# Optimization experiments

Measured on AMD Instinct MI355X. Metric: run time of the kernel, lower is better.

Reference implementation:

```python
import jax, jax.numpy as jnp
import numpy as np

B, C, H, W = 32, 128, 32, 32
E, K, D, HID = 16, 2, 128, 512  # nbExperts, topK, nbIn=nbOut, hidden=4*max(nbIn,nbOut)


def setup_inputs() -> dict:
    key = jax.random.key(0)
    ks = jax.random.split(key, 6)
    init = lambda k, shape, fan: (jax.random.normal(k, shape, jnp.float32) / np.sqrt(fan)).astype(jnp.float32)
    return {
        "x": jax.random.normal(ks[0], (B, C, H, W), jnp.float32),
        "gate_w": init(ks[1], (D, E), D),
        "gate_b": jnp.zeros((E,), jnp.float32),
        "noise_w": init(ks[2], (D, E), D),
        "noise_b": jnp.zeros((E,), jnp.float32),
        "w1": init(ks[3], (E, D, HID), D),
        "b1": jnp.zeros((E, HID), jnp.float32),
        "w2": init(ks[4], (E, HID, D), HID),
        "b2": jnp.zeros((E, D), jnp.float32),
        "top_k": K,
    }


def reference(x, gate_w, gate_b, noise_w, noise_b, w1, b1, w2, b2, top_k):
    b, c, h, w = x.shape
    xt = x.transpose(0, 2, 3, 1).reshape(-1, c)  # [T, D] tokens (fromCNN path)
    T = xt.shape[0]

    # --- GatingWithNoise: gate(x) + randn * softplus(noise(x)) ---
    logits = xt @ gate_w + gate_b                      # [T, E]
    noise_sd = jax.nn.softplus(xt @ noise_w + noise_b)  # [T, E]
    noise = jax.random.normal(jax.random.key(42), logits.shape, logits.dtype)
    logits = logits + noise * noise_sd

    # --- top-k, softmax over k, scatter to dense [T, E] gate matrix ---
    top_vals, top_idx = jax.lax.top_k(logits, top_k)   # [T, K]
    probs = jax.nn.softmax(top_vals, axis=1)           # [T, K]
    gates = jnp.zeros((T, E), x.dtype).at[jnp.arange(T)[:, None], top_idx].set(probs)

    # --- dense path: run every expert, weighted combine ---
    hdn = jax.nn.relu(jnp.einsum('td,edh->teh', xt, w1) + b1)  # [T, E, HID]
    eo = jnp.einsum('teh,ehd->ted', hdn, w2) + b2              # [T, E, D]
    out = jnp.einsum('te,ted->td', gates, eo)                  # [T, D]

    out = out.reshape(b, h, w, c).transpose(0, 3, 1, 2)        # back to NCHW
    gates = gates.reshape(b, h, w, E)
    return out, gates
```

## Files before the change

### kernel.cpp

```cpp
#include <hip/hip_runtime.h>
#include <stdint.h>

#define NB       32
#define NC       128
#define NHW      1024
#define NT       32768
#define NE       16
#define NHID     512
#define NGBLK    512

typedef __attribute__((ext_vector_type(8))) short short8v;
typedef __attribute__((ext_vector_type(4))) float f32x4;

__device__ __forceinline__ unsigned short f2bf(float f) {
    uint32_t u = __float_as_uint(f);
    uint32_t r = u + 0x7fffu + ((u >> 16) & 1u);
    return (unsigned short)(r >> 16);
}
__device__ __forceinline__ float bf2f(unsigned short u) {
    return __uint_as_float(((uint32_t)u) << 16);
}

__device__ __forceinline__ void gll16(const void* g, void* l) {
    __builtin_amdgcn_global_load_lds(
        (const __attribute__((address_space(1))) uint32_t*)g,
        (__attribute__((address_space(3))) uint32_t*)l, 16, 0, 0);
}

#define WAIT_VM4_LGKM0() asm volatile("s_waitcnt vmcnt(4) lgkmcnt(0)" ::: "memory")
#define WAIT_VM0_LGKM0() asm volatile("s_waitcnt vmcnt(0) lgkmcnt(0)" ::: "memory")
#define WAIT_LGKM()      asm volatile("s_waitcnt lgkmcnt(0)" ::: "memory")
#define SBAR()           { asm volatile("" ::: "memory"); __builtin_amdgcn_s_barrier(); asm volatile("" ::: "memory"); }

__device__ __forceinline__ uint32_t rotl32(uint32_t x, uint32_t d) {
    return (x << d) | (x >> (32u - d));
}

__device__ __forceinline__ void threefry2x32_20(uint32_t k0, uint32_t k1,
                                                uint32_t& x0, uint32_t& x1) {
    const uint32_t ks0 = k0, ks1 = k1, ks2 = k0 ^ k1 ^ 0x1BD11BDAu;
    x0 += ks0; x1 += ks1;
#define TFR(r) { x0 += x1; x1 = rotl32(x1, r); x1 ^= x0; }
    TFR(13u) TFR(15u) TFR(26u) TFR(6u)
    x0 += ks1; x1 += ks2 + 1u;
    TFR(17u) TFR(29u) TFR(16u) TFR(24u)
    x0 += ks2; x1 += ks0 + 2u;
    TFR(13u) TFR(15u) TFR(26u) TFR(6u)
    x0 += ks0; x1 += ks1 + 3u;
    TFR(17u) TFR(29u) TFR(16u) TFR(24u)
    x0 += ks1; x1 += ks2 + 4u;
    TFR(13u) TFR(15u) TFR(26u) TFR(6u)
    x0 += ks2; x1 += ks0 + 5u;
#undef TFR
}

__device__ __forceinline__ float erfinv_xla_f32(float x) {
    float w = -log1pf(-x * x);
    float p;
    if (w < 5.0f) {
        w = w - 2.5f;
        p = 2.81022636e-08f;
        p = fmaf(p, w, 3.43273939e-07f);
        p = fmaf(p, w, -3.5233877e-06f);
        p = fmaf(p, w, -4.39150654e-06f);
        p = fmaf(p, w, 0.00021858087f);
        p = fmaf(p, w, -0.00125372503f);
        p = fmaf(p, w, -0.00417768164f);
        p = fmaf(p, w, 0.246640727f);
        p = fmaf(p, w, 1.50140941f);
    } else {
        w = sqrtf(w) - 3.0f;
        p = -0.000200214257f;
        p = fmaf(p, w, 0.000100950558f);
        p = fmaf(p, w, 0.00134934322f);
        p = fmaf(p, w, -0.00367342844f);
        p = fmaf(p, w, 0.00573950773f);
        p = fmaf(p, w, -0.0076224613f);
        p = fmaf(p, w, 0.00943887047f);
        p = fmaf(p, w, 1.00167406f);
        p = fmaf(p, w, 2.83297682f);
    }
    return p * x;
}

__device__ __forceinline__ float jax_noise_elem(uint32_t i) {
    uint32_t x0 = 0u, x1 = i;
    threefry2x32_20(0u, 42u, x0, x1);
    uint32_t bits = x0 ^ x1;
    float f = __uint_as_float(0x3f800000u | (bits >> 9)) - 1.0f;
    const float lo = -0.99999994f;
    float u = f * 2.0f + lo;
    u = fmaxf(lo, u);
    return 1.41421354f * erfinv_xla_f32(u);
}

__global__ __launch_bounds__(256) void moe_gate_tw_kernel(
    const float* __restrict__ x,
    const float* __restrict__ gate_w, const float* __restrict__ gate_b,
    const float* __restrict__ noise_w, const float* __restrict__ noise_b,
    float* __restrict__ gates_out,
    int*   __restrict__ top_idx,
    float* __restrict__ top_prob,
    int*   __restrict__ rank,
    int*   __restrict__ bcnt,
    unsigned short* __restrict__ xtb,
    const float* __restrict__ w1, unsigned short* __restrict__ w1bt,
    const float* __restrict__ w2, unsigned short* __restrict__ w2bt,
    int do_new)
{
    __shared__ union { float lw[32 * 160]; float ts[64][65]; } sm;
    __shared__ int lcnt[16];

    const int tid = threadIdx.x;

    if (blockIdx.x >= NGBLK) {
        int blk = blockIdx.x - NGBLK;
        const float* src;  unsigned short* dst;  int R, C;
        if (blk < 256) { src = w1; dst = w1bt; R = 128; C = 512; }
        else           { src = w2; dst = w2bt; R = 512; C = 128; blk -= 256; }
        const int nr = R >> 6, ncc = C >> 6;
        const int e = blk / (nr * ncc);
        const int rem = blk % (nr * ncc);
        const int rt = rem / ncc, ct = rem % ncc;
        const float* S = src + (size_t)e * R * C + (size_t)(rt * 64) * C + ct * 64;
        unsigned short* D = dst + (size_t)e * R * C + (size_t)(ct * 64) * R + rt * 64;
        #pragma unroll
        for (int i = 0; i < 16; ++i) {
            int lin = i * 256 + tid;
            int r = lin >> 6, c = lin & 63;
            sm.ts[r][c] = S[(size_t)r * C + c];
        }
        __syncthreads();
        #pragma unroll
        for (int i = 0; i < 16; ++i) {
            int lin = i * 256 + tid;
            int c = lin >> 6, r = lin & 63;
            D[(size_t)c * R + r] = f2bf(sm.ts[r][c]);
        }
        return;
    }

    const int tl  = tid >> 2;
    const int q   = tid & 3;
    const int t   = blockIdx.x * 64 + tl;
    const int b   = t >> 10, hw = t & 1023;

    if (tid < 16) lcnt[tid] = 0;

    for (int idx = tid; idx < 4096; idx += 256) {
        int ci = idx >> 7;
        int r  = idx & 127;
        int qq = r >> 5, e = r & 31;
        int c  = qq * 32 + ci;
        float v = (e < 16) ? gate_w[c * 16 + e] : noise_w[c * 16 + (e - 16)];
        sm.lw[ci * 160 + qq * 40 + e] = v;
    }
    __syncthreads();

    float acc[32];
    #pragma unroll
    for (int e = 0; e < 32; ++e) acc[e] = 0.f;

    unsigned short xh[32];
    const float* xq = x + (size_t)b * (NC * NHW) + (size_t)(q * 32) * NHW + hw;
    const float* wq = sm.lw + q * 40;
    #pragma unroll 4
    for (int ci = 0; ci < 32; ++ci) {
        float xv = xq[(size_t)ci << 10];
        xh[ci] = f2bf(xv);
        const f32x4* wr = (const f32x4*)(wq + ci * 160);
        #pragma unroll
        for (int j = 0; j < 8; ++j) {
            f32x4 w4 = wr[j];
            #pragma unroll
            for (int k = 0; k < 4; ++k)
                acc[j * 4 + k] = fmaf(xv, w4[k], acc[j * 4 + k]);
        }
    }

    if (do_new) {
        #pragma unroll
        for (int j = 0; j < 4; ++j) {
            short8v v;
            #pragma unroll
            for (int k = 0; k < 8; ++k) v[k] = (short)xh[j * 8 + k];
            *(short8v*)(xtb + (size_t)t * 128 + q * 32 + j * 8) = v;
        }
    }

    #pragma unroll
    for (int e = 0; e < 32; ++e) {
        acc[e] += __shfl_xor(acc[e], 1);
        acc[e] += __shfl_xor(acc[e], 2);
    }

    float lg[4];
    #pragma unroll
    for (int j = 0; j < 4; ++j) {
        int e = q * 4 + j;
        float g  = acc[e] + gate_b[e];
        float an = acc[16 + e] + noise_b[e];
        float sd = fmaxf(an, 0.f) + log1pf(expf(-fabsf(an)));
        float nz = jax_noise_elem((uint32_t)t * 16u + (uint32_t)e);
        lg[j] = fmaf(nz, sd, g);
    }

    float v1 = lg[0], v2 = -INFINITY;
    int   i1 = q * 4, i2 = 0x7fffffff;
    #pragma unroll
    for (int j = 1; j < 4; ++j) {
        float v = lg[j]; int e = q * 4 + j;
        if (v > v1) { v2 = v1; i2 = i1; v1 = v; i1 = e; }
        else if (v > v2) { v2 = v; i2 = e; }
    }
    #pragma unroll
    for (int m = 1; m <= 2; m <<= 1) {
        float pv1 = __shfl_xor(v1, m), pv2 = __shfl_xor(v2, m);
        int   pi1 = __shfl_xor(i1, m), pi2 = __shfl_xor(i2, m);
        bool pBest = (pv1 > v1) || (pv1 == v1 && pi1 < i1);
        float c2v; int c2i;
        if (pBest) { c2v = v1;  c2i = i1;  v1 = pv1; i1 = pi1;
                     if (!((c2v > pv2) || (c2v == pv2 && c2i < pi2))) { c2v = pv2; c2i = pi2; }
        } else     { c2v = pv1; c2i = pi1;
                     if (!((c2v > v2)  || (c2v == v2  && c2i < i2)))  { c2v = v2;  c2i = i2;  }
        }
        v2 = c2v; i2 = c2i;
    }

    float qq = expf(v2 - v1);
    float s  = 1.0f + qq;
    float p1 = 1.0f / s;
    float p2 = qq / s;

    f32x4 g4;
    #pragma unroll
    for (int j = 0; j < 4; ++j) {
        int e = q * 4 + j;
        g4[j] = (e == i1) ? p1 : ((e == i2) ? p2 : 0.f);
    }
    *(f32x4*)(gates_out + (size_t)t * 16 + q * 4) = g4;

    if (q == 0) {
        top_idx[t * 2 + 0] = i1;  top_idx[t * 2 + 1] = i2;
        top_prob[t * 2 + 0] = p1; top_prob[t * 2 + 1] = p2;
        if (do_new) {
            int r1 = atomicAdd(&lcnt[i1], 1);
            int r2 = atomicAdd(&lcnt[i2], 1);
            rank[t * 2 + 0] = r1;
            rank[t * 2 + 1] = r2;
        }
    }
    if (do_new) {
        __syncthreads();
        if (tid < 16) bcnt[blockIdx.x * 16 + tid] = lcnt[tid];
    }
}

__global__ __launch_bounds__(256) void scan_kernel(
    const int* __restrict__ bcnt,
    int* __restrict__ poff, int* __restrict__ blk2e,
    int* __restrict__ blk2chunk, int* __restrict__ total_chunks,
    int* __restrict__ bbase,
    int* __restrict__ pair_tok)
{
    __shared__ int ps[16][17];
    __shared__ int gb[16][17];
    __shared__ int scnt[16];
    __shared__ int snch[16];
    __shared__ int scum[17];
    __shared__ int spoff[16];
    const int tid = threadIdx.x;
    const int e = tid >> 4, g = tid & 15;

    int s = 0;
    for (int b = g * 32; b < g * 32 + 32; ++b)
        s += bcnt[b * 16 + e];
    ps[e][g] = s;
    __syncthreads();

    if (tid < 16) {
        int run = 0;
        for (int gg = 0; gg < 16; ++gg) { gb[tid][gg] = run; run += ps[tid][gg]; }
        scnt[tid] = run;
        snch[tid] = (run + 127) >> 7;
    }
    __syncthreads();

    if (tid == 0) {
        int cc = 0, off = 0;
        for (int ee = 0; ee < 16; ++ee) {
            scum[ee] = cc; spoff[ee] = off;
            cc += snch[ee]; off += snch[ee] << 7;
        }
        scum[16] = cc;
        *total_chunks = cc;
    }
    __syncthreads();
    const int tot = scum[16];
    for (int idx = tid; idx < tot; idx += 256) {
        int ee = 0;
        #pragma unroll
        for (int k = 0; k < 15; ++k)
            if (idx >= scum[k + 1]) ee = k + 1;
        blk2e[idx] = ee;
        blk2chunk[idx] = idx - scum[ee];
    }
    if (tid < 16) poff[tid] = spoff[tid];

    {
        int run = spoff[e] + gb[e][g];
        for (int b = g * 32; b < g * 32 + 32; ++b) {
            bbase[b * 16 + e] = run;
            run += bcnt[b * 16 + e];
        }
    }

    for (int ee = 0; ee < 16; ++ee) {
        int start = spoff[ee] + scnt[ee];
        int end   = spoff[ee] + (snch[ee] << 7);
        for (int i = start + tid; i < end; i += 256)
            pair_tok[i] = -1;
    }
}

__global__ __launch_bounds__(256) void scatter_kernel(
    const int* __restrict__ top_idx, const int* __restrict__ rank,
    const int* __restrict__ bbase, int* __restrict__ pair_tok,
    int* __restrict__ slot_of)
{
    int i = blockIdx.x * 256 + threadIdx.x;
    int t = i >> 1;
    int e = top_idx[i];
    int slot = bbase[(t >> 6) * 16 + e] + rank[i];
    pair_tok[slot] = t;
    slot_of[i] = slot;
}

__device__ __forceinline__ void stage_w1(const unsigned short* w1e, short* W1s,
                                         int hcn, int wid, int lane) {
    #pragma unroll
    for (int k2 = 0; k2 < 2; ++k2) {
        int i2 = wid * 2 + k2;
        int r2 = i2 * 4 + (lane >> 4);
        int s2 = lane & 15;
        gll16(w1e + (size_t)(hcn + r2) * 128 + ((s2 ^ (r2 & 15)) * 8),
              W1s + i2 * 512);
    }
}
__device__ __forceinline__ void stage_w2(const unsigned short* w2e, short* W2s,
                                         int hcn, int wid, int lane) {
    #pragma unroll
    for (int k2 = 0; k2 < 2; ++k2) {
        int i2 = wid * 2 + k2;
        int r2 = i2 * 8 + (lane >> 3);
        int s2 = lane & 7;
        gll16(w2e + (size_t)r2 * 512 + hcn + ((s2 ^ (r2 & 7)) * 8),
              W2s + i2 * 512);
    }
}

__global__ __launch_bounds__(512, 4) void moe_mfma_kernel(
    const unsigned short* __restrict__ xtb,
    const int* __restrict__ pair_tok, const int* __restrict__ blk2e,
    const int* __restrict__ blk2chunk, const int* __restrict__ poff,
    const int* __restrict__ total_chunks,
    const unsigned short* __restrict__ w1bt,
    const float* __restrict__ b1,
    const unsigned short* __restrict__ w2bt,
    const float* __restrict__ b2,
    unsigned short* __restrict__ pair_y)
{
    __shared__ short Hs[128 * 64];
    __shared__ short W1s[2][64 * 128];
    __shared__ short W2s[2][128 * 64];

    const int blk = (blockIdx.x & 7) * 66 + (blockIdx.x >> 3);
    if (blk >= *total_chunks) return;
    const int e  = blk2e[blk];
    const int p0 = poff[e] + (blk2chunk[blk] << 7);
    const int tid  = threadIdx.x;
    const int lane = tid & 63;
    const int wid  = tid >> 6;
    const int wm   = wid >> 1;
    const int wn   = wid & 1;
    const int l16  = lane & 15;
    const int lg   = lane >> 4;

    const unsigned short* w1e = w1bt + (size_t)e * 512 * 128;
    const unsigned short* w2e = w2bt + (size_t)e * 128 * 512;

    short8v xa[2][4];
    #pragma unroll
    for (int af = 0; af < 2; ++af) {
        int row = wm * 32 + af * 16 + l16;
        int tok = pair_tok[p0 + row];
        #pragma unroll
        for (int kk = 0; kk < 4; ++kk) {
            short8v v = {};
            if (tok >= 0)
                v = *(const short8v*)(xtb + (size_t)tok * 128 + kk * 32 + lg * 8);
            xa[af][kk] = v;
        }
    }

    stage_w1(w1e, W1s[0], 0, wid, lane);
    stage_w2(w2e, W2s[0], 0, wid, lane);
    stage_w1(w1e, W1s[1], 64, wid, lane);
    stage_w2(w2e, W2s[1], 64, wid, lane);

    f32x4 yacc[2][4];
    #pragma unroll
    for (int af = 0; af < 2; ++af)
        #pragma unroll
        for (int nj = 0; nj < 4; ++nj)
            yacc[af][nj] = (f32x4){0.f, 0.f, 0.f, 0.f};

    const int rowA0 = wm * 32 + l16, rowA1 = rowA0 + 16;

    for (int c = 0; c < 8; ++c) {
        const short* W1b = W1s[c & 1];
        const short* W2b = W2s[c & 1];

        if (c >= 1 && c <= 6) {
            stage_w1(w1e, W1s[(c + 1) & 1], (c + 1) << 6, wid, lane);
            stage_w2(w2e, W2s[(c + 1) & 1], (c + 1) << 6, wid, lane);
        }
        if (c <= 6) { WAIT_VM4_LGKM0(); } else { WAIT_VM0_LGKM0(); }
        SBAR();

        f32x4 hacc[2][2];
        #pragma unroll
        for (int af = 0; af < 2; ++af)
            #pragma unroll
            for (int ni = 0; ni < 2; ++ni)
                hacc[af][ni] = (f32x4){0.f, 0.f, 0.f, 0.f};

        __builtin_amdgcn_s_setprio(1);
        #pragma unroll
        for (int kk = 0; kk < 4; ++kk) {
            int slot = kk * 4 + lg;
            #pragma unroll
            for (int ni = 0; ni < 2; ++ni) {
                int hr = wn * 32 + ni * 16 + l16;
                short8v bfr = *(const short8v*)(W1b + hr * 128 + ((slot ^ (hr & 15)) * 8));
                #pragma unroll
                for (int af = 0; af < 2; ++af)
                    hacc[af][ni] = __builtin_amdgcn_mfma_f32_16x16x32_bf16(
                        xa[af][kk], bfr, hacc[af][ni], 0, 0, 0);
            }
        }
        __builtin_amdgcn_s_setprio(0);

        #pragma unroll
        for (int ni = 0; ni < 2; ++ni) {
            int col = wn * 32 + ni * 16 + l16;
            float b1v = b1[e * 512 + (c << 6) + col];
            #pragma unroll
            for (int af = 0; af < 2; ++af) {
                #pragma unroll
                for (int r = 0; r < 4; ++r) {
                    int m = wm * 32 + af * 16 + lg * 4 + r;
                    float v = fmaxf(hacc[af][ni][r] + b1v, 0.f);
                    Hs[m * 64 + (((col >> 3) ^ (m & 7)) << 3) + (col & 7)] = (short)f2bf(v);
                }
            }
        }
        WAIT_LGKM(); SBAR();

        __builtin_amdgcn_s_setprio(1);
        #pragma unroll
        for (int kk = 0; kk < 2; ++kk) {
            int slot = kk * 4 + lg;
            short8v a0 = *(const short8v*)(Hs + rowA0 * 64 + ((slot ^ (rowA0 & 7)) * 8));
            short8v a1 = *(const short8v*)(Hs + rowA1 * 64 + ((slot ^ (rowA1 & 7)) * 8));
            #pragma unroll
            for (int nj = 0; nj < 4; ++nj) {
                int dr = wn * 64 + nj * 16 + l16;
                short8v bfr = *(const short8v*)(W2b + dr * 64 + ((slot ^ (dr & 7)) * 8));
                yacc[0][nj] = __builtin_amdgcn_mfma_f32_16x16x32_bf16(a0, bfr, yacc[0][nj], 0, 0, 0);
                yacc[1][nj] = __builtin_amdgcn_mfma_f32_16x16x32_bf16(a1, bfr, yacc[1][nj], 0, 0, 0);
            }
        }
        __builtin_amdgcn_s_setprio(0);
        WAIT_LGKM(); SBAR();
    }

    #pragma unroll
    for (int nj = 0; nj < 4; ++nj) {
        int d = wn * 64 + nj * 16 + l16;
        float b2v = b2[e * 128 + d];
        #pragma unroll
        for (int af = 0; af < 2; ++af) {
            #pragma unroll
            for (int r = 0; r < 4; ++r) {
                int m = wm * 32 + af * 16 + lg * 4 + r;
                pair_y[(size_t)(p0 + m) * 128 + d] = f2bf(yacc[af][nj][r] + b2v);
            }
        }
    }
}

__global__ __launch_bounds__(256) void combine_kernel(
    const unsigned short* __restrict__ pair_y, const int* __restrict__ slot_of,
    const float* __restrict__ top_prob, float* __restrict__ out)
{
    __shared__ float ob[64][129];
    const int blk = blockIdx.x;
    const int b = blk >> 4;
    const int hw0 = (blk & 15) << 6;
    const int tid = threadIdx.x;
    #pragma unroll
    for (int i = 0; i < 4; ++i) {
        int lin = i * 256 + tid;
        int tl = lin >> 4, dg = lin & 15;
        int t = b * 1024 + hw0 + tl;
        int s0 = slot_of[t * 2], s1 = slot_of[t * 2 + 1];
        float p0 = top_prob[t * 2], p1 = top_prob[t * 2 + 1];
        short8v y0 = *(const short8v*)(pair_y + (size_t)s0 * 128 + dg * 8);
        short8v y1 = *(const short8v*)(pair_y + (size_t)s1 * 128 + dg * 8);
        #pragma unroll
        for (int j = 0; j < 8; ++j)
            ob[tl][dg * 8 + j] = p0 * bf2f((unsigned short)y0[j]) + p1 * bf2f((unsigned short)y1[j]);
    }
    __syncthreads();
    #pragma unroll
    for (int i = 0; i < 32; ++i) {
        int lin = i * 256 + tid;
        int d = lin >> 6, hwl = lin & 63;
        out[((size_t)b * 128 + d) * 1024 + hw0 + hwl] = ob[hwl][d];
    }
}

__global__ __launch_bounds__(256) void moe_expert_kernel(
    const float* __restrict__ x,
    const int* __restrict__ top_idx, const float* __restrict__ top_prob,
    const float* __restrict__ w1, const float* __restrict__ b1,
    const float* __restrict__ w2, const float* __restrict__ b2,
    float* __restrict__ out)
{
    __shared__ float xsB[128];
    __shared__ float hb[512];

    const int tid = threadIdx.x;
    const int t = blockIdx.x;
    const int b = t >> 10, hw = t & 1023;

    if (tid < 128)
        xsB[tid] = x[((size_t)b * 128 + tid) * NHW + hw];
    __syncthreads();

    float oacc = 0.f;
    #pragma unroll
    for (int k = 0; k < 2; ++k) {
        const int e = top_idx[t * 2 + k];
        const float pw = top_prob[t * 2 + k];
        const float* W1 = w1 + (size_t)e * (128 * 512);
        float a0 = 0.f, a1 = 0.f;
        for (int d = 0; d < 128; ++d) {
            float xv = xsB[d];
            a0 = fmaf(xv, W1[d * 512 + tid], a0);
            a1 = fmaf(xv, W1[d * 512 + tid + 256], a1);
        }
        hb[tid]       = fmaxf(a0 + b1[e * 512 + tid], 0.f);
        hb[tid + 256] = fmaxf(a1 + b1[e * 512 + tid + 256], 0.f);
        __syncthreads();
        if (tid < 128) {
            const float* W2 = w2 + (size_t)e * (512 * 128);
            float a = 0.f;
            for (int h = 0; h < 512; ++h)
                a = fmaf(hb[h], W2[h * 128 + tid], a);
            oacc = fmaf(pw, a + b2[e * 128 + tid], oacc);
        }
        __syncthreads();
    }
    if (tid < 128)
        out[((size_t)b * 128 + tid) * NHW + hw] = oacc;
}

extern "C" void kernel_launch(void* const* d_in, const int* in_sizes, int n_in,
                              void* d_out, int out_size, void* d_ws, size_t ws_size,
                              hipStream_t stream) {
    const float* x       = (const float*)d_in[0];
    const float* gate_w  = (const float*)d_in[1];
    const float* gate_b  = (const float*)d_in[2];
    const float* noise_w = (const float*)d_in[3];
    const float* noise_b = (const float*)d_in[4];
    const float* w1      = (const float*)d_in[5];
    const float* b1      = (const float*)d_in[6];
    const float* w2      = (const float*)d_in[7];
    const float* b2      = (const float*)d_in[8];

    float* out   = (float*)d_out;
    float* gates = out + (size_t)NB * NC * NHW;

    const size_t OFF_POFF   = 0;
    const size_t OFF_TOTAL  = 1024;
    const size_t OFF_B2E    = 4096;
    const size_t OFF_B2C    = 8192;
    const size_t OFF_TIDX   = 12288;
    const size_t OFF_RANK   = OFF_TIDX  + (size_t)NT * 2 * 4;
    const size_t OFF_SLOT   = OFF_RANK  + (size_t)NT * 2 * 4;
    const size_t OFF_PROB   = OFF_SLOT  + (size_t)NT * 2 * 4;
    const size_t OFF_BCNT   = OFF_PROB  + (size_t)NT * 2 * 4;
    const size_t OFF_BBASE  = OFF_BCNT  + (size_t)NGBLK * 16 * 4;
    const size_t OFF_XTB    = OFF_BBASE + (size_t)NGBLK * 16 * 4;
    const size_t OFF_W1BT   = OFF_XTB   + (size_t)NT * 128 * 2;
    const size_t OFF_W2BT   = OFF_W1BT  + (size_t)NE * 512 * 128 * 2;
    const size_t OFF_PTOK   = OFF_W2BT  + (size_t)NE * 128 * 512 * 2;
    const size_t NPAIR_PAD  = 67584;
    const size_t OFF_PAIRY  = OFF_PTOK  + NPAIR_PAD * 4;
    const size_t NEED       = OFF_PAIRY + NPAIR_PAD * 128 * 2;

    char* ws = (char*)d_ws;
    int*   poff     = (int*)(ws + OFF_POFF);
    int*   total_ch = (int*)(ws + OFF_TOTAL);
    int*   blk2e    = (int*)(ws + OFF_B2E);
    int*   blk2c    = (int*)(ws + OFF_B2C);
    int*   top_idx  = (int*)(ws + OFF_TIDX);
    int*   rank     = (int*)(ws + OFF_RANK);
    int*   slot_of  = (int*)(ws + OFF_SLOT);
    float* top_prob = (float*)(ws + OFF_PROB);
    int*   bcnt     = (int*)(ws + OFF_BCNT);
    int*   bbase    = (int*)(ws + OFF_BBASE);
    unsigned short* xtb    = (unsigned short*)(ws + OFF_XTB);
    unsigned short* w1bt   = (unsigned short*)(ws + OFF_W1BT);
    unsigned short* w2bt   = (unsigned short*)(ws + OFF_W2BT);
    int*   pair_tok = (int*)(ws + OFF_PTOK);
    unsigned short* pair_y = (unsigned short*)(ws + OFF_PAIRY);

    const int use_new = (ws_size >= NEED) ? 1 : 0;

    moe_gate_tw_kernel<<<use_new ? (NGBLK + 512) : NGBLK, 256, 0, stream>>>(
        x, gate_w, gate_b, noise_w, noise_b,
        gates, top_idx, top_prob, rank, bcnt, xtb,
        w1, w1bt, w2, w2bt, use_new);

    if (use_new) {
        scan_kernel<<<1, 256, 0, stream>>>(bcnt, poff, blk2e, blk2c, total_ch,
                                           bbase, pair_tok);
        scatter_kernel<<<NT * 2 / 256, 256, 0, stream>>>(top_idx, rank, bbase,
                                                         pair_tok, slot_of);
        moe_mfma_kernel<<<528, 512, 0, stream>>>(
            xtb, pair_tok, blk2e, blk2c, poff, total_ch,
            w1bt, b1, w2bt, b2, pair_y);
        combine_kernel<<<512, 256, 0, stream>>>(pair_y, slot_of, top_prob, out);
    } else {
        moe_expert_kernel<<<NT, 256, 0, stream>>>(
            x, top_idx, top_prob, w1, b1, w2, b2, out);
    }
}
```

Baseline: 98.80 us.

## Single-buffer expert weights, swap MFMA operands, and vectorize hidden-tile LDS stores

Drops the double-buffered W1/W2 LDS staging in favour of single buffers. Each buffer is refilled for the next chunk only after the stage that reads it has passed a barrier. This cuts LDS per block, which may allow more resident blocks. The warp layout changes to 2x4, and the first GEMM swaps operands (weights as A, tokens as B) so each lane holds 4 consecutive hidden values. That lets bias be loaded as a float4 and the hidden tile be written to LDS as packed 8-byte stores instead of scalar shorts. The cost is less overlap between weight loads and compute, since every chunk now waits on vmcnt(0).

```diff
diff --git a/kernel.cpp b/kernel.cpp
--- a/kernel.cpp
+++ b/kernel.cpp
@@ -11,6 +11,7 @@
 
 typedef __attribute__((ext_vector_type(8))) short short8v;
 typedef __attribute__((ext_vector_type(4))) float f32x4;
+typedef __attribute__((ext_vector_type(2))) uint32_t uint2v;
 
 __device__ __forceinline__ unsigned short f2bf(float f) {
     uint32_t u = __float_as_uint(f);
@@ -27,7 +28,6 @@
         (__attribute__((address_space(3))) uint32_t*)l, 16, 0, 0);
 }
 
-#define WAIT_VM4_LGKM0() asm volatile("s_waitcnt vmcnt(4) lgkmcnt(0)" ::: "memory")
 #define WAIT_VM0_LGKM0() asm volatile("s_waitcnt vmcnt(0) lgkmcnt(0)" ::: "memory")
 #define WAIT_LGKM()      asm volatile("s_waitcnt lgkmcnt(0)" ::: "memory")
 #define SBAR()           { asm volatile("" ::: "memory"); __builtin_amdgcn_s_barrier(); asm volatile("" ::: "memory"); }
@@ -371,8 +371,8 @@
     unsigned short* __restrict__ pair_y)
 {
     __shared__ short Hs[128 * 64];
-    __shared__ short W1s[2][64 * 128];
-    __shared__ short W2s[2][128 * 64];
+    __shared__ short W1s[64 * 128];
+    __shared__ short W2s[128 * 64];
 
     const int blk = (blockIdx.x & 7) * 66 + (blockIdx.x >> 3);
     if (blk >= *total_chunks) return;
@@ -381,32 +381,30 @@
     const int tid  = threadIdx.x;
     const int lane = tid & 63;
     const int wid  = tid >> 6;
-    const int wm   = wid >> 1;
-    const int wn   = wid & 1;
+    const int wm   = wid >> 2;
+    const int wn   = wid & 3;
     const int l16  = lane & 15;
     const int lg   = lane >> 4;
 
     const unsigned short* w1e = w1bt + (size_t)e * 512 * 128;
     const unsigned short* w2e = w2bt + (size_t)e * 128 * 512;
 
+    stage_w1(w1e, W1s, 0, wid, lane);
+    stage_w2(w2e, W2s, 0, wid, lane);
+
     short8v xa[2][4];
     #pragma unroll
-    for (int af = 0; af < 2; ++af) {
-        int row = wm * 32 + af * 16 + l16;
+    for (int ni = 0; ni < 2; ++ni) {
+        int row = wn * 32 + ni * 16 + l16;
         int tok = pair_tok[p0 + row];
         #pragma unroll
         for (int kk = 0; kk < 4; ++kk) {
             short8v v = {};
             if (tok >= 0)
                 v = *(const short8v*)(xtb + (size_t)tok * 128 + kk * 32 + lg * 8);
-            xa[af][kk] = v;
-        }
-    }
-
-    stage_w1(w1e, W1s[0], 0, wid, lane);
-    stage_w2(w2e, W2s[0], 0, wid, lane);
-    stage_w1(w1e, W1s[1], 64, wid, lane);
-    stage_w2(w2e, W2s[1], 64, wid, lane);
+            xa[ni][kk] = v;
+        }
+    }
 
     f32x4 yacc[2][4];
     #pragma unroll
@@ -415,57 +413,55 @@
         for (int nj = 0; nj < 4; ++nj)
             yacc[af][nj] = (f32x4){0.f, 0.f, 0.f, 0.f};
 
-    const int rowA0 = wm * 32 + l16, rowA1 = rowA0 + 16;
+    const int rowA0 = wn * 32 + l16, rowA1 = rowA0 + 16;
 
     for (int c = 0; c < 8; ++c) {
-        const short* W1b = W1s[c & 1];
-        const short* W2b = W2s[c & 1];
-
-        if (c >= 1 && c <= 6) {
-            stage_w1(w1e, W1s[(c + 1) & 1], (c + 1) << 6, wid, lane);
-            stage_w2(w2e, W2s[(c + 1) & 1], (c + 1) << 6, wid, lane);
-        }
-        if (c <= 6) { WAIT_VM4_LGKM0(); } else { WAIT_VM0_LGKM0(); }
-        SBAR();
+        WAIT_VM0_LGKM0(); SBAR();
 
         f32x4 hacc[2][2];
         #pragma unroll
-        for (int af = 0; af < 2; ++af)
+        for (int mi = 0; mi < 2; ++mi)
             #pragma unroll
             for (int ni = 0; ni < 2; ++ni)
-                hacc[af][ni] = (f32x4){0.f, 0.f, 0.f, 0.f};
+                hacc[mi][ni] = (f32x4){0.f, 0.f, 0.f, 0.f};
 
         __builtin_amdgcn_s_setprio(1);
         #pragma unroll
         for (int kk = 0; kk < 4; ++kk) {
             int slot = kk * 4 + lg;
             #pragma unroll
+            for (int mi = 0; mi < 2; ++mi) {
+                int hr = wm * 32 + mi * 16 + l16;
+                short8v wfr = *(const short8v*)(W1s + hr * 128 + ((slot ^ (hr & 15)) * 8));
+                #pragma unroll
+                for (int ni = 0; ni < 2; ++ni)
+                    hacc[mi][ni] = __builtin_amdgcn_mfma_f32_16x16x32_bf16(
+                        wfr, xa[ni][kk], hacc[mi][ni], 0, 0, 0);
+            }
+        }
+        __builtin_amdgcn_s_setprio(0);
+
+        #pragma unroll
+        for (int mi = 0; mi < 2; ++mi) {
+            int h0 = wm * 32 + mi * 16 + lg * 4;
+            f32x4 b1v = *(const f32x4*)(b1 + e * 512 + (c << 6) + h0);
+            #pragma unroll
             for (int ni = 0; ni < 2; ++ni) {
-                int hr = wn * 32 + ni * 16 + l16;
-                short8v bfr = *(const short8v*)(W1b + hr * 128 + ((slot ^ (hr & 15)) * 8));
-                #pragma unroll
-                for (int af = 0; af < 2; ++af)
-                    hacc[af][ni] = __builtin_amdgcn_mfma_f32_16x16x32_bf16(
-                        xa[af][kk], bfr, hacc[af][ni], 0, 0, 0);
+                int tok = wn * 32 + ni * 16 + l16;
+                float v0 = fmaxf(hacc[mi][ni][0] + b1v[0], 0.f);
+                float v1 = fmaxf(hacc[mi][ni][1] + b1v[1], 0.f);
+                float v2 = fmaxf(hacc[mi][ni][2] + b1v[2], 0.f);
+                float v3 = fmaxf(hacc[mi][ni][3] + b1v[3], 0.f);
+                uint32_t lo = (uint32_t)f2bf(v0) | ((uint32_t)f2bf(v1) << 16);
+                uint32_t hi = (uint32_t)f2bf(v2) | ((uint32_t)f2bf(v3) << 16);
+                int slot = h0 >> 3;
+                int addr = tok * 64 + ((slot ^ (tok & 7)) << 3) + (h0 & 7);
+                *(uint2v*)(Hs + addr) = (uint2v){lo, hi};
             }
         }
-        __builtin_amdgcn_s_setprio(0);
-
-        #pragma unroll
-        for (int ni = 0; ni < 2; ++ni) {
-            int col = wn * 32 + ni * 16 + l16;
-            float b1v = b1[e * 512 + (c << 6) + col];
-            #pragma unroll
-            for (int af = 0; af < 2; ++af) {
-                #pragma unroll
-                for (int r = 0; r < 4; ++r) {
-                    int m = wm * 32 + af * 16 + lg * 4 + r;
-                    float v = fmaxf(hacc[af][ni][r] + b1v, 0.f);
-                    Hs[m * 64 + (((col >> 3) ^ (m & 7)) << 3) + (col & 7)] = (short)f2bf(v);
-                }
-            }
-        }
         WAIT_LGKM(); SBAR();
+
+        if (c < 7) stage_w1(w1e, W1s, (c + 1) << 6, wid, lane);
 
         __builtin_amdgcn_s_setprio(1);
         #pragma unroll
@@ -475,25 +471,27 @@
             short8v a1 = *(const short8v*)(Hs + rowA1 * 64 + ((slot ^ (rowA1 & 7)) * 8));
             #pragma unroll
             for (int nj = 0; nj < 4; ++nj) {
-                int dr = wn * 64 + nj * 16 + l16;
-                short8v bfr = *(const short8v*)(W2b + dr * 64 + ((slot ^ (dr & 7)) * 8));
+                int dr = wm * 64 + nj * 16 + l16;
+                short8v bfr = *(const short8v*)(W2s + dr * 64 + ((slot ^ (dr & 7)) * 8));
                 yacc[0][nj] = __builtin_amdgcn_mfma_f32_16x16x32_bf16(a0, bfr, yacc[0][nj], 0, 0, 0);
                 yacc[1][nj] = __builtin_amdgcn_mfma_f32_16x16x32_bf16(a1, bfr, yacc[1][nj], 0, 0, 0);
             }
         }
         __builtin_amdgcn_s_setprio(0);
         WAIT_LGKM(); SBAR();
+
+        if (c < 7) stage_w2(w2e, W2s, (c + 1) << 6, wid, lane);
     }
 
     #pragma unroll
     for (int nj = 0; nj < 4; ++nj) {
-        int d = wn * 64 + nj * 16 + l16;
+        int d = wm * 64 + nj * 16 + l16;
         float b2v = b2[e * 128 + d];
         #pragma unroll
         for (int af = 0; af < 2; ++af) {
             #pragma unroll
             for (int r = 0; r < 4; ++r) {
-                int m = wm * 32 + af * 16 + lg * 4 + r;
+                int m = wn * 32 + af * 16 + lg * 4 + r;
                 pair_y[(size_t)(p0 + m) * 128 + d] = f2bf(yacc[af][nj][r] + b2v);
             }
         }
```

Measured after the change: 94.09 us. 1.05x faster.
